# Performance work log

Measured on AMD Instinct MI355X. Metric: run time of the kernel, lower is better.

The kernel has to match this reference:

```python
import jax, jax.numpy as jnp
import numpy as np

B, N, M, Wlen = 4, 20000, 64, 8


def setup_inputs() -> dict:
    key = jax.random.key(0)
    k1, k2, k3, k4 = jax.random.split(key, 4)
    a0 = jax.random.uniform(k1, (B, N), dtype=jnp.float32)
    W = 0.01 * jax.random.normal(k2, (M, M), dtype=jnp.float32)
    X1 = jax.random.randint(k3, (M, N, Wlen, 2), 0, N, dtype=jnp.int64)
    X2 = jax.random.randint(k4, (M, N, Wlen, 2), 0, N, dtype=jnp.int64)
    return {"a0": a0, "W": W, "X1": X1, "X2": X2, "T": 2}


def f_clause_stack(a, X):
    # a: [B,n], X: [m,n,w,2] -> [B,m,n]
    y1 = a[:, X[..., 0]]  # [B,m,n,w] gather
    y2 = a[:, X[..., 1]]
    return jnp.max(y1 * y2, axis=3)


def predicate_forward(a, W, X1, X2, temperature=1.0):
    F1 = f_clause_stack(a, X1)  # [B,m1,n]
    F2 = f_clause_stack(a, X2)  # [B,m2,n]
    pi = jax.nn.softmax((W / temperature).reshape(-1)).reshape(W.shape)  # [m1,m2]
    pi1 = pi.sum(axis=1)  # [m1]
    pi2 = pi.sum(axis=0)  # [m2]
    Eu = jnp.einsum('j,bjn->bn', pi1, F1)
    Ev = jnp.einsum('k,bkn->bn', pi2, F2)
    Mt = jnp.einsum('jk,bkn->bjn', pi, F2)
    Euv = jnp.sum(F1 * Mt, axis=1)
    return Eu + Ev - Euv  # [B,n]


def reference(a0, W, X1, X2, T):
    a = a0
    for _ in range(T):  # T is a small static int
        derived = predicate_forward(a, W, X1, X2)
        # single intensional predicate -> stack/max over predicates is identity
        a = 1.0 - (1.0 - a) * (1.0 - derived)
    return a
```

## Files before the change

kernel.cpp:

```cpp
#include <hip/hip_runtime.h>

#define NN 20000

typedef _Float16 f16x2 __attribute__((ext_vector_type(2)));
typedef unsigned short u16x2 __attribute__((ext_vector_type(2)));

union U32H2 { unsigned int u; f16x2 h; };
union U32S2 { unsigned int u; u16x2 s; };

__device__ __forceinline__ f16x2 bc_h2(unsigned int u) { U32H2 x; x.u = u; return x.h; }
__device__ __forceinline__ unsigned int dup_h(float v) {
    _Float16 h = (_Float16)v;
    unsigned short b = __builtin_bit_cast(unsigned short, h);
    return ((unsigned int)b << 16) | b;
}
__device__ __forceinline__ unsigned int pkrtz_u32(float a, float b) {
    return __builtin_bit_cast(unsigned int, __builtin_amdgcn_cvt_pkrtz(a, b));
}

template <int CTRL>
__device__ __forceinline__ unsigned int pkmax_dpp(unsigned int v) {
    unsigned int d = (unsigned int)__builtin_amdgcn_update_dpp(
        0, (int)v, CTRL, 0xF, 0xF, true);
    U32S2 a, b; a.u = v; b.u = d;
    a.s = __builtin_elementwise_max(a.s, b.s);
    return a.u;
}
__device__ __forceinline__ unsigned int octmax_u16x2(unsigned int v) {
    v = pkmax_dpp<0xB1>(v);
    v = pkmax_dpp<0x4E>(v);
    v = pkmax_dpp<0x141>(v);
    return v;
}

__global__ __launch_bounds__(1024) void prep_kernel(const float* __restrict__ W,
                                                    unsigned int* __restrict__ pi_pk,
                                                    unsigned int* __restrict__ pi_t_pk,
                                                    unsigned int* __restrict__ pi1_pk,
                                                    unsigned int* __restrict__ pi2_pk) {
    __shared__ float red[1024];
    __shared__ float piL[4096];
    int t = threadIdx.x;
    float4 wv = ((const float4*)W)[t];
    float m = fmaxf(fmaxf(wv.x, wv.y), fmaxf(wv.z, wv.w));
    red[t] = m; __syncthreads();
    for (int s = 512; s > 0; s >>= 1) {
        if (t < s) red[t] = fmaxf(red[t], red[t + s]);
        __syncthreads();
    }
    m = red[0];
    __syncthreads();
    float e0 = expf(wv.x - m), e1 = expf(wv.y - m);
    float e2 = expf(wv.z - m), e3 = expf(wv.w - m);
    red[t] = e0 + e1 + e2 + e3;
    __syncthreads();
    for (int s = 512; s > 0; s >>= 1) {
        if (t < s) red[t] += red[t + s];
        __syncthreads();
    }
    float inv = 1.0f / red[0];
    float p[4] = { e0 * inv, e1 * inv, e2 * inv, e3 * inv };
#pragma unroll
    for (int i = 0; i < 4; i++) {
        int f = t * 4 + i;
        piL[f] = p[i];
        unsigned int d = dup_h(p[i]);
        pi_pk[f] = d;
        pi_t_pk[(f & 63) * 64 + (f >> 6)] = d;
    }
    __syncthreads();
    if (t < 64) {
        float s = 0.f;
        for (int k = 0; k < 64; k++) s += piL[t * 64 + k];
        pi1_pk[t] = dup_h(s);
    } else if (t < 128) {
        int k = t - 64;
        float s = 0.f;
        for (int j = 0; j < 64; j++) s += piL[j * 64 + k];
        pi2_pk[k] = dup_h(s);
    }
}

__global__ __launch_bounds__(1024) void pack_kernel(const float* __restrict__ a0,
                                                    unsigned int* __restrict__ T0) {
    int i = blockIdx.x * 1024 + threadIdx.x;
    if (i < NN) {
        unsigned int b0 = __float2uint_rn(__saturatef(a0[i]) * 255.0f);
        unsigned int b1 = __float2uint_rn(__saturatef(a0[NN + i]) * 255.0f);
        unsigned int b2 = __float2uint_rn(__saturatef(a0[2 * NN + i]) * 255.0f);
        unsigned int b3 = __float2uint_rn(__saturatef(a0[3 * NN + i]) * 255.0f);
        T0[i] = b0 | (b1 << 8) | (b2 << 16) | (b3 << 24);
    }
}

template <int ITER>
__global__ __launch_bounds__(1024, 4) void fused_iter(
    const unsigned int* __restrict__ Tsrc,
    const int* __restrict__ X1, const int* __restrict__ X2,
    const unsigned int* __restrict__ pi_t_pk,
    const unsigned int* __restrict__ pi1_pk,
    const unsigned int* __restrict__ pi2_pk,
    const float* __restrict__ a0,
    unsigned int* __restrict__ Tdst, float* __restrict__ outP) {
    __shared__ unsigned int tab[NN];
    __shared__ unsigned int Ft[128][40][2];
    __shared__ float redp[8][64][4];
    __shared__ float a_sm[64][4];

    const int t = threadIdx.x;
    for (int i = t; i < NN; i += 1024) tab[i] = Tsrc[i];

    const int bid = (int)blockIdx.x;
    const int bstart = bid < 32 ? bid * 79 : 32 * 79 + (bid - 32) * 78;
    const int bcnt = bid < 32 ? 79 : 78;
    const int c0 = (bcnt + 1) >> 1;

    const int wid = t >> 6, lane = t & 63, ni = lane >> 3, w = lane & 7;
    const int q = t >> 7, bp = (t >> 6) & 1, n_l = t & 63;
    const int widu = __builtin_amdgcn_readfirstlane(wid);
    const int qu = __builtin_amdgcn_readfirstlane(q);

    __syncthreads();

    for (int ch = 0; ch < 2; ++ch) {
        const int nb = bstart + (ch ? c0 : 0);
        const int cn = ch ? (bcnt - c0) : c0;

        {
            const float sc = 1.0f / 65025.0f;
            int loff[5];
#pragma unroll
            for (int oc = 0; oc < 5; ++oc) {
                int n = nb + oc * 8 + ni;
                int nc = n < NN ? n : NN - 1;
                loff[oc] = nc * 64 + w * 8;
            }
            int2 q5[5];
            {
                const int row = widu, k = row & 63;
                const char* Xb = (const char*)((row >> 6) ? X2 : X1)
                               + (unsigned)(k * NN) * 64u;
#pragma unroll
                for (int oc = 0; oc < 5; ++oc)
                    q5[oc] = *(const int2*)(Xb + loff[oc]);
            }
#pragma unroll
            for (int rr = 0; rr < 8; ++rr) {
                int2 qn[5];
                if (rr < 7) {
                    const int row = widu + 16 * (rr + 1), k = row & 63;
                    const char* Xb = (const char*)((row >> 6) ? X2 : X1)
                                   + (unsigned)(k * NN) * 64u;
#pragma unroll
                    for (int oc = 0; oc < 5; ++oc)
                        qn[oc] = *(const int2*)(Xb + loff[oc]);
                }
                const int row = widu + 16 * rr;
                unsigned int ga[5], gb[5];
#pragma unroll
                for (int oc = 0; oc < 5; ++oc) {
                    ga[oc] = tab[q5[oc].x];
                    gb[oc] = tab[q5[oc].y];
                }
#pragma unroll
                for (int oc = 0; oc < 5; ++oc) {
                    unsigned int ea = ga[oc] & 0x00FF00FFu;
                    unsigned int oa = (ga[oc] >> 8) & 0x00FF00FFu;
                    unsigned int eb = gb[oc] & 0x00FF00FFu;
                    unsigned int ob = (gb[oc] >> 8) & 0x00FF00FFu;
                    U32S2 pe, po, xb;
                    pe.u = ea; xb.u = eb; pe.s = pe.s * xb.s;
                    po.u = oa; xb.u = ob; po.s = po.s * xb.s;
                    unsigned int peu = octmax_u16x2(pe.u);
                    unsigned int pou = octmax_u16x2(po.u);
                    int col = oc * 8 + ni;
                    if (w == 0 && col < cn) {
                        float f0 = (float)(peu & 0xFFFFu) * sc;
                        float f1 = (float)(pou & 0xFFFFu) * sc;
                        float f2 = (float)(peu >> 16) * sc;
                        float f3 = (float)(pou >> 16) * sc;
                        unsigned int ul = pkrtz_u32(f0, f1);
                        unsigned int uh = pkrtz_u32(f2, f3);
                        *(uint2*)&Ft[row][col][0] = make_uint2(ul, uh);
                    }
                }
#pragma unroll
                for (int oc = 0; oc < 5; ++oc) q5[oc] = qn[oc];
            }
        }
        __syncthreads();

        {
            float part0 = 0.f, part1 = 0.f;
            if (n_l < cn) {
                f16x2 zero = {(_Float16)0, (_Float16)0};
                f16x2 f1v[8];
                f16x2 eu = zero;
#pragma unroll
                for (int jj = 0; jj < 8; ++jj) {
                    f1v[jj] = bc_h2(Ft[qu * 8 + jj][n_l][bp]);
                    eu += bc_h2(pi1_pk[qu * 8 + jj]) * f1v[jj];
                }
                f16x2 euv = zero, ev = zero;
#pragma unroll 8
                for (int k = 0; k < 64; ++k) {
                    f16x2 f2 = bc_h2(Ft[64 + k][n_l][bp]);
                    const uint4* pt = (const uint4*)(pi_t_pk + k * 64 + qu * 8);
                    uint4 w0 = pt[0], w1 = pt[1];
                    f16x2 ts = bc_h2(w0.x) * f1v[0] + bc_h2(w0.y) * f1v[1] +
                               bc_h2(w0.z) * f1v[2] + bc_h2(w0.w) * f1v[3] +
                               bc_h2(w1.x) * f1v[4] + bc_h2(w1.y) * f1v[5] +
                               bc_h2(w1.z) * f1v[6] + bc_h2(w1.w) * f1v[7];
                    euv += f2 * ts;
                    if (qu == 0) ev += bc_h2(pi2_pk[k]) * f2;
                }
                part0 = (float)eu[0] - (float)euv[0];
                part1 = (float)eu[1] - (float)euv[1];
                if (qu == 0) {
                    part0 += (float)ev[0];
                    part1 += (float)ev[1];
                }
            }
            *(float2*)&redp[q][n_l][bp * 2] = make_float2(part0, part1);
        }
        __syncthreads();

        if (t < 256) {
            int n = t & 63, b = t >> 6;
            if (n < cn) {
                float d = 0.f;
#pragma unroll
                for (int q8 = 0; q8 < 8; ++q8) d += redp[q8][n][b];
                int gn = nb + n;
                float ap;
                if (ITER == 1) ap = a0[(size_t)b * NN + gn];
                else ap = (float)((tab[gn] >> (8 * b)) & 255u) * (1.0f / 255.0f);
                float an = 1.0f - (1.0f - ap) * (1.0f - d);
                if (ITER == 1) a_sm[n][b] = an;
                else outP[(size_t)b * NN + gn] = an;
            }
        }
        __syncthreads();
        if (ITER == 1 && t < 64 && t < cn) {
            unsigned int b0 = __float2uint_rn(__saturatef(a_sm[t][0]) * 255.0f);
            unsigned int b1 = __float2uint_rn(__saturatef(a_sm[t][1]) * 255.0f);
            unsigned int b2 = __float2uint_rn(__saturatef(a_sm[t][2]) * 255.0f);
            unsigned int b3 = __float2uint_rn(__saturatef(a_sm[t][3]) * 255.0f);
            Tdst[nb + t] = b0 | (b1 << 8) | (b2 << 16) | (b3 << 24);
        }
        __syncthreads();
    }
}

extern "C" void kernel_launch(void* const* d_in, const int* in_sizes, int n_in,
                              void* d_out, int out_size, void* d_ws, size_t ws_size,
                              hipStream_t stream) {
    const float* a0 = (const float*)d_in[0];
    const float* W = (const float*)d_in[1];
    const int* X1 = (const int*)d_in[2];
    const int* X2 = (const int*)d_in[3];
    float* out = (float*)d_out;

    if (ws_size < (size_t)193280) return;
    unsigned int* pi_pk  = (unsigned int*)d_ws;
    unsigned int* pi_t   = (unsigned int*)((char*)d_ws + 16384);
    unsigned int* pi1_pk = (unsigned int*)((char*)d_ws + 32768);
    unsigned int* pi2_pk = (unsigned int*)((char*)d_ws + 33024);
    unsigned int* T0     = (unsigned int*)((char*)d_ws + 33280);
    unsigned int* T1     = (unsigned int*)((char*)d_ws + 113280);

    prep_kernel<<<1, 1024, 0, stream>>>(W, pi_pk, pi_t, pi1_pk, pi2_pk);
    pack_kernel<<<20, 1024, 0, stream>>>(a0, T0);
    fused_iter<1><<<256, 1024, 0, stream>>>(T0, X1, X2, pi_t, pi1_pk, pi2_pk,
                                            a0, T1, nullptr);
    fused_iter<2><<<256, 1024, 0, stream>>>(T1, X1, X2, pi_t, pi1_pk, pi2_pk,
                                            nullptr, nullptr, out);
}
```

Baseline: 249.0 us.

## Double-buffer clause tiles to overlap gather of next chunk with contraction

Each block's columns are split into three 32-column chunks instead of two of about 40. The Ft tile and the reduction buffer are double-buffered, so the gather/max phase for chunk c+1 runs in the same barrier interval as the pi-weighted contraction for chunk c. The final update step is also merged so one thread handles all four batch entries, which removes the a_sm staging buffer and two barriers per chunk. In exchange, half of the threads have no column to work on during the contraction phase, and there is one extra chunk of gather work with padded columns.

```diff
diff --git a/kernel.cpp b/kernel.cpp
--- a/kernel.cpp
+++ b/kernel.cpp
@@ -1,6 +1,7 @@
 #include <hip/hip_runtime.h>
 
 #define NN 20000
+#define COLS 32
 
 typedef _Float16 f16x2 __attribute__((ext_vector_type(2)));
 typedef unsigned short u16x2 __attribute__((ext_vector_type(2)));
@@ -93,6 +94,98 @@
     }
 }
 
+__device__ __forceinline__ void phase1(
+    const unsigned int* __restrict__ tab,
+    unsigned int (* __restrict__ Ftb)[COLS][2],
+    const int* __restrict__ X1, const int* __restrict__ X2,
+    int nb, int cn, int widu, int ni, int w) {
+    const float sc = 1.0f / 65025.0f;
+    int loff[4];
+#pragma unroll
+    for (int oc = 0; oc < 4; ++oc) {
+        int n = nb + oc * 8 + ni;
+        int nc = n < NN ? n : NN - 1;
+        loff[oc] = nc * 64 + w * 8;
+    }
+    int2 q5[4];
+    {
+        const int row = widu, k = row & 63;
+        const char* Xb = (const char*)((row >> 6) ? X2 : X1) + (unsigned)(k * NN) * 64u;
+#pragma unroll
+        for (int oc = 0; oc < 4; ++oc) q5[oc] = *(const int2*)(Xb + loff[oc]);
+    }
+#pragma unroll
+    for (int rr = 0; rr < 8; ++rr) {
+        int2 qn[4];
+        if (rr < 7) {
+            const int row = widu + 16 * (rr + 1), k = row & 63;
+            const char* Xb = (const char*)((row >> 6) ? X2 : X1) + (unsigned)(k * NN) * 64u;
+#pragma unroll
+            for (int oc = 0; oc < 4; ++oc) qn[oc] = *(const int2*)(Xb + loff[oc]);
+        }
+        const int row = widu + 16 * rr;
+        unsigned int ga[4], gb[4];
+#pragma unroll
+        for (int oc = 0; oc < 4; ++oc) { ga[oc] = tab[q5[oc].x]; gb[oc] = tab[q5[oc].y]; }
+#pragma unroll
+        for (int oc = 0; oc < 4; ++oc) {
+            unsigned int ea = ga[oc] & 0x00FF00FFu;
+            unsigned int oa = (ga[oc] >> 8) & 0x00FF00FFu;
+            unsigned int eb = gb[oc] & 0x00FF00FFu;
+            unsigned int ob = (gb[oc] >> 8) & 0x00FF00FFu;
+            U32S2 pe, po, xb;
+            pe.u = ea; xb.u = eb; pe.s = pe.s * xb.s;
+            po.u = oa; xb.u = ob; po.s = po.s * xb.s;
+            unsigned int peu = octmax_u16x2(pe.u);
+            unsigned int pou = octmax_u16x2(po.u);
+            int col = oc * 8 + ni;
+            if (w == 0 && col < cn) {
+                float f0 = (float)(peu & 0xFFFFu) * sc;
+                float f1 = (float)(pou & 0xFFFFu) * sc;
+                float f2 = (float)(peu >> 16) * sc;
+                float f3 = (float)(pou >> 16) * sc;
+                *(uint2*)&Ftb[row][col][0] =
+                    make_uint2(pkrtz_u32(f0, f1), pkrtz_u32(f2, f3));
+            }
+        }
+#pragma unroll
+        for (int oc = 0; oc < 4; ++oc) q5[oc] = qn[oc];
+    }
+}
+
+__device__ __forceinline__ float2 phase2(
+    const unsigned int (* __restrict__ Ftb)[COLS][2],
+    const unsigned int* __restrict__ pi_t_pk,
+    const unsigned int* __restrict__ pi1_pk,
+    const unsigned int* __restrict__ pi2_pk,
+    int qu, int bp, int n_l) {
+    f16x2 zero = {(_Float16)0, (_Float16)0};
+    f16x2 f1v[8];
+    f16x2 eu = zero;
+#pragma unroll
+    for (int jj = 0; jj < 8; ++jj) {
+        f1v[jj] = bc_h2(Ftb[qu * 8 + jj][n_l][bp]);
+        eu += bc_h2(pi1_pk[qu * 8 + jj]) * f1v[jj];
+    }
+    f16x2 euv = zero, ev = zero;
+#pragma unroll 8
+    for (int k = 0; k < 64; ++k) {
+        f16x2 f2 = bc_h2(Ftb[64 + k][n_l][bp]);
+        const uint4* pt = (const uint4*)(pi_t_pk + k * 64 + qu * 8);
+        uint4 w0 = pt[0], w1 = pt[1];
+        f16x2 ts = bc_h2(w0.x) * f1v[0] + bc_h2(w0.y) * f1v[1] +
+                   bc_h2(w0.z) * f1v[2] + bc_h2(w0.w) * f1v[3] +
+                   bc_h2(w1.x) * f1v[4] + bc_h2(w1.y) * f1v[5] +
+                   bc_h2(w1.z) * f1v[6] + bc_h2(w1.w) * f1v[7];
+        euv += f2 * ts;
+        if (qu == 0) ev += bc_h2(pi2_pk[k]) * f2;
+    }
+    float p0 = (float)eu[0] - (float)euv[0];
+    float p1 = (float)eu[1] - (float)euv[1];
+    if (qu == 0) { p0 += (float)ev[0]; p1 += (float)ev[1]; }
+    return make_float2(p0, p1);
+}
+
 template <int ITER>
 __global__ __launch_bounds__(1024, 4) void fused_iter(
     const unsigned int* __restrict__ Tsrc,
@@ -103,9 +196,8 @@
     const float* __restrict__ a0,
     unsigned int* __restrict__ Tdst, float* __restrict__ outP) {
     __shared__ unsigned int tab[NN];
-    __shared__ unsigned int Ft[128][40][2];
-    __shared__ float redp[8][64][4];
-    __shared__ float a_sm[64][4];
+    __shared__ unsigned int Ft[2][128][COLS][2];
+    __shared__ float redp[2][8][COLS][4];
 
     const int t = threadIdx.x;
     for (int i = t; i < NN; i += 1024) tab[i] = Tsrc[i];
@@ -113,7 +205,8 @@
     const int bid = (int)blockIdx.x;
     const int bstart = bid < 32 ? bid * 79 : 32 * 79 + (bid - 32) * 78;
     const int bcnt = bid < 32 ? 79 : 78;
-    const int c0 = (bcnt + 1) >> 1;
+    const int nbs[3] = { bstart, bstart + 32, bstart + 64 };
+    const int cns[3] = { 32, 32, bcnt - 64 };
 
     const int wid = t >> 6, lane = t & 63, ni = lane >> 3, w = lane & 7;
     const int q = t >> 7, bp = (t >> 6) & 1, n_l = t & 63;
@@ -121,134 +214,56 @@
     const int qu = __builtin_amdgcn_readfirstlane(q);
 
     __syncthreads();
-
-    for (int ch = 0; ch < 2; ++ch) {
-        const int nb = bstart + (ch ? c0 : 0);
-        const int cn = ch ? (bcnt - c0) : c0;
-
-        {
-            const float sc = 1.0f / 65025.0f;
-            int loff[5];
-#pragma unroll
-            for (int oc = 0; oc < 5; ++oc) {
-                int n = nb + oc * 8 + ni;
-                int nc = n < NN ? n : NN - 1;
-                loff[oc] = nc * 64 + w * 8;
-            }
-            int2 q5[5];
-            {
-                const int row = widu, k = row & 63;
-                const char* Xb = (const char*)((row >> 6) ? X2 : X1)
-                               + (unsigned)(k * NN) * 64u;
-#pragma unroll
-                for (int oc = 0; oc < 5; ++oc)
-                    q5[oc] = *(const int2*)(Xb + loff[oc]);
-            }
-#pragma unroll
-            for (int rr = 0; rr < 8; ++rr) {
-                int2 qn[5];
-                if (rr < 7) {
-                    const int row = widu + 16 * (rr + 1), k = row & 63;
-                    const char* Xb = (const char*)((row >> 6) ? X2 : X1)
-                                   + (unsigned)(k * NN) * 64u;
-#pragma unroll
-                    for (int oc = 0; oc < 5; ++oc)
-                        qn[oc] = *(const int2*)(Xb + loff[oc]);
-                }
-                const int row = widu + 16 * rr;
-                unsigned int ga[5], gb[5];
-#pragma unroll
-                for (int oc = 0; oc < 5; ++oc) {
-                    ga[oc] = tab[q5[oc].x];
-                    gb[oc] = tab[q5[oc].y];
-                }
-#pragma unroll
-                for (int oc = 0; oc < 5; ++oc) {
-                    unsigned int ea = ga[oc] & 0x00FF00FFu;
-                    unsigned int oa = (ga[oc] >> 8) & 0x00FF00FFu;
-                    unsigned int eb = gb[oc] & 0x00FF00FFu;
-                    unsigned int ob = (gb[oc] >> 8) & 0x00FF00FFu;
-                    U32S2 pe, po, xb;
-                    pe.u = ea; xb.u = eb; pe.s = pe.s * xb.s;
-                    po.u = oa; xb.u = ob; po.s = po.s * xb.s;
-                    unsigned int peu = octmax_u16x2(pe.u);
-                    unsigned int pou = octmax_u16x2(po.u);
-                    int col = oc * 8 + ni;
-                    if (w == 0 && col < cn) {
-                        float f0 = (float)(peu & 0xFFFFu) * sc;
-                        float f1 = (float)(pou & 0xFFFFu) * sc;
-                        float f2 = (float)(peu >> 16) * sc;
-                        float f3 = (float)(pou >> 16) * sc;
-                        unsigned int ul = pkrtz_u32(f0, f1);
-                        unsigned int uh = pkrtz_u32(f2, f3);
-                        *(uint2*)&Ft[row][col][0] = make_uint2(ul, uh);
-                    }
-                }
-#pragma unroll
-                for (int oc = 0; oc < 5; ++oc) q5[oc] = qn[oc];
-            }
-        }
+    phase1(tab, Ft[0], X1, X2, nbs[0], cns[0], widu, ni, w);
+    __syncthreads();
+
+    for (int c = 0; c < 3; ++c) {
+        const int cur = c & 1;
+        if (n_l < cns[c]) {
+            float2 pp = phase2(Ft[cur], pi_t_pk, pi1_pk, pi2_pk, qu, bp, n_l);
+            *(float2*)&redp[cur][q][n_l][bp * 2] = pp;
+        }
+        if (c < 2)
+            phase1(tab, Ft[cur ^ 1], X1, X2, nbs[c + 1], cns[c + 1], widu, ni, w);
         __syncthreads();
-
-        {
-            float part0 = 0.f, part1 = 0.f;
-            if (n_l < cn) {
-                f16x2 zero = {(_Float16)0, (_Float16)0};
-                f16x2 f1v[8];
-                f16x2 eu = zero;
-#pragma unroll
-                for (int jj = 0; jj < 8; ++jj) {
-                    f1v[jj] = bc_h2(Ft[qu * 8 + jj][n_l][bp]);
-                    eu += bc_h2(pi1_pk[qu * 8 + jj]) * f1v[jj];
-                }
-                f16x2 euv = zero, ev = zero;
-#pragma unroll 8
-                for (int k = 0; k < 64; ++k) {
-                    f16x2 f2 = bc_h2(Ft[64 + k][n_l][bp]);
-                    const uint4* pt = (const uint4*)(pi_t_pk + k * 64 + qu * 8);
-                    uint4 w0 = pt[0], w1 = pt[1];
-                    f16x2 ts = bc_h2(w0.x) * f1v[0] + bc_h2(w0.y) * f1v[1] +
-                               bc_h2(w0.z) * f1v[2] + bc_h2(w0.w) * f1v[3] +
-                               bc_h2(w1.x) * f1v[4] + bc_h2(w1.y) * f1v[5] +
-                               bc_h2(w1.z) * f1v[6] + bc_h2(w1.w) * f1v[7];
-                    euv += f2 * ts;
-                    if (qu == 0) ev += bc_h2(pi2_pk[k]) * f2;
-                }
-                part0 = (float)eu[0] - (float)euv[0];
-                part1 = (float)eu[1] - (float)euv[1];
-                if (qu == 0) {
-                    part0 += (float)ev[0];
-                    part1 += (float)ev[1];
-                }
-            }
-            *(float2*)&redp[q][n_l][bp * 2] = make_float2(part0, part1);
-        }
-        __syncthreads();
-
-        if (t < 256) {
-            int n = t & 63, b = t >> 6;
-            if (n < cn) {
-                float d = 0.f;
-#pragma unroll
-                for (int q8 = 0; q8 < 8; ++q8) d += redp[q8][n][b];
-                int gn = nb + n;
-                float ap;
-                if (ITER == 1) ap = a0[(size_t)b * NN + gn];
-                else ap = (float)((tab[gn] >> (8 * b)) & 255u) * (1.0f / 255.0f);
-                float an = 1.0f - (1.0f - ap) * (1.0f - d);
-                if (ITER == 1) a_sm[n][b] = an;
-                else outP[(size_t)b * NN + gn] = an;
-            }
-        }
-        __syncthreads();
-        if (ITER == 1 && t < 64 && t < cn) {
-            unsigned int b0 = __float2uint_rn(__saturatef(a_sm[t][0]) * 255.0f);
-            unsigned int b1 = __float2uint_rn(__saturatef(a_sm[t][1]) * 255.0f);
-            unsigned int b2 = __float2uint_rn(__saturatef(a_sm[t][2]) * 255.0f);
-            unsigned int b3 = __float2uint_rn(__saturatef(a_sm[t][3]) * 255.0f);
-            Tdst[nb + t] = b0 | (b1 << 8) | (b2 << 16) | (b3 << 24);
-        }
-        __syncthreads();
+        if (t < cns[c]) {
+            int gn = nbs[c] + t;
+            float d0 = 0.f, d1 = 0.f, d2 = 0.f, d3 = 0.f;
+#pragma unroll
+            for (int q8 = 0; q8 < 8; ++q8) {
+                d0 += redp[cur][q8][t][0];
+                d1 += redp[cur][q8][t][1];
+                d2 += redp[cur][q8][t][2];
+                d3 += redp[cur][q8][t][3];
+            }
+            float ap0, ap1, ap2, ap3;
+            if (ITER == 1) {
+                ap0 = a0[gn]; ap1 = a0[NN + gn];
+                ap2 = a0[2 * NN + gn]; ap3 = a0[3 * NN + gn];
+            } else {
+                unsigned int tv = tab[gn];
+                ap0 = (float)(tv & 255u) * (1.0f / 255.0f);
+                ap1 = (float)((tv >> 8) & 255u) * (1.0f / 255.0f);
+                ap2 = (float)((tv >> 16) & 255u) * (1.0f / 255.0f);
+                ap3 = (float)(tv >> 24) * (1.0f / 255.0f);
+            }
+            float an0 = 1.0f - (1.0f - ap0) * (1.0f - d0);
+            float an1 = 1.0f - (1.0f - ap1) * (1.0f - d1);
+            float an2 = 1.0f - (1.0f - ap2) * (1.0f - d2);
+            float an3 = 1.0f - (1.0f - ap3) * (1.0f - d3);
+            if (ITER == 1) {
+                unsigned int b0 = __float2uint_rn(__saturatef(an0) * 255.0f);
+                unsigned int b1 = __float2uint_rn(__saturatef(an1) * 255.0f);
+                unsigned int b2 = __float2uint_rn(__saturatef(an2) * 255.0f);
+                unsigned int b3 = __float2uint_rn(__saturatef(an3) * 255.0f);
+                Tdst[gn] = b0 | (b1 << 8) | (b2 << 16) | (b3 << 24);
+            } else {
+                outP[gn] = an0;
+                outP[NN + gn] = an1;
+                outP[2 * NN + gn] = an2;
+                outP[3 * NN + gn] = an3;
+            }
+        }
     }
 }
 
```

After: 258.2 us. 3.7% more time.
